# Kernel optimization log

Measured on AMD Instinct MI355X. Metric: run time of the kernel, lower is better.

## Reference

```python
import jax, jax.numpy as jnp
import numpy as np
import math

E = 256          # embed_dim
H = 8            # num_heads
DH = E // H      # head_dim = 32
Q_LEN = 65536
KV_LEN = 65536
K_NBR = 16       # max_memory_len (neighbors per query)


def setup_inputs() -> dict:
    key = jax.random.key(0)
    ks = jax.random.split(key, 8)
    query = jax.random.normal(ks[0], (Q_LEN, E), dtype=jnp.float32)
    key_t = jax.random.normal(ks[1], (KV_LEN, E), dtype=jnp.float32)
    value = jax.random.normal(ks[2], (KV_LEN, E), dtype=jnp.float32)
    index_pair = jax.random.randint(ks[3], (Q_LEN, K_NBR), 0, KV_LEN, dtype=jnp.int64 if jax.config.jax_enable_x64 else jnp.int32)
    # learned params (xavier-ish init for in_proj, zero biases)
    lim = math.sqrt(6.0 / (3 * E + E))
    in_proj_weight = jax.random.uniform(ks[4], (3 * E, E), minval=-lim, maxval=lim, dtype=jnp.float32)
    in_proj_bias = jnp.zeros((3 * E,), dtype=jnp.float32)
    lim2 = math.sqrt(1.0 / E)
    out_proj_weight = jax.random.uniform(ks[5], (E, E), minval=-lim2, maxval=lim2, dtype=jnp.float32)
    out_proj_bias = jnp.zeros((E,), dtype=jnp.float32)
    return {
        "query": query, "key": key_t, "value": value, "index_pair": index_pair,
        "in_proj_weight": in_proj_weight, "in_proj_bias": in_proj_bias,
        "out_proj_weight": out_proj_weight, "out_proj_bias": out_proj_bias,
    }


def reference(query, key, value, index_pair, in_proj_weight, in_proj_bias, out_proj_weight, out_proj_bias):
    tq = query.shape[0]
    # input projections (split rows of packed in_proj_weight)
    q = query @ in_proj_weight[:E].T + in_proj_bias[:E]
    k = key @ in_proj_weight[E:2 * E].T + in_proj_bias[E:2 * E]
    v = value @ in_proj_weight[2 * E:].T + in_proj_bias[2 * E:]
    q = q.reshape(tq, H, DH) / math.sqrt(DH)   # [Q,H,Dh]
    k = k.reshape(-1, H, DH)                    # [N,H,Dh]
    v = v.reshape(-1, H, DH)
    invalid = index_pair < 0                    # [Q,K]
    all_invalid = jnp.all(invalid, axis=-1)     # [Q]
    safe_pair = jnp.clip(index_pair, 0)
    gathered_k = k[safe_pair]                   # [Q,K,H,Dh]
    gathered_v = v[safe_pair]
    weights = jnp.einsum('qhd,qkhd->qkh', q, gathered_k)  # [Q,K,H]
    neg_inf = jnp.asarray(-jnp.inf, weights.dtype)
    weights = jnp.where(invalid[..., None], neg_inf, weights)
    weights = jnp.where(all_invalid[:, None, None], jnp.zeros((), weights.dtype), weights)
    weights = jax.nn.softmax(weights, axis=1)
    weights = jnp.where(invalid[..., None], jnp.zeros((), weights.dtype), weights)
    out = jnp.einsum('qkh,qkhd->qhd', weights, gathered_v).reshape(tq, E)
    out = out @ out_proj_weight.T + out_proj_bias
    return out, weights.sum(axis=-1) / H
```

## Files before the change

kernel.cpp:

```cpp
#include <hip/hip_runtime.h>
#include <hip/hip_fp16.h>

#define QLEN   65536
#define EDIM   256

typedef _Float16 half8 __attribute__((ext_vector_type(8)));
typedef float    f32x4 __attribute__((ext_vector_type(4)));

static const size_t WQKV_OFF = 0;
static const size_t WOUT_OFF = 768u * 256u * 2u;
static const size_t Q_OFF    = WOUT_OFF + 256u * 256u * 2u;
static const size_t K_OFF    = Q_OFF + (size_t)QLEN * EDIM * 2u;
static const size_t V_OFF    = K_OFF + (size_t)QLEN * EDIM * 2u;
static const size_t A_OFF    = V_OFF + (size_t)QLEN * EDIM * 2u;

__global__ void prep_weights(const float* __restrict__ wqkv,
                             const float* __restrict__ wout,
                             __half* __restrict__ dst)
{
  int g = (blockIdx.x * blockDim.x + threadIdx.x) * 4;
  float4 f;
  if (g < 768 * 256) f = *(const float4*)(wqkv + g);
  else               f = *(const float4*)(wout + (g - 768 * 256));
  union { __half h[4]; uint2 u; } c;
  c.h[0] = __float2half(f.x); c.h[1] = __float2half(f.y);
  c.h[2] = __float2half(f.z); c.h[3] = __float2half(f.w);
  *(uint2*)(dst + g) = c.u;
}

template<bool A_F32, bool OUT_F16>
__global__ __launch_bounds__(512)
void gemm_e256v2(const void* __restrict__ A0, const void* __restrict__ A1,
                 const void* __restrict__ A2,
                 const __half* __restrict__ Wbase, const float* __restrict__ bias,
                 float scale0,
                 void* __restrict__ O0, void* __restrict__ O1, void* __restrict__ O2)
{
  __shared__ __half As[2][128][40];
  __shared__ __half Bs[2][256][40];

  const int y = blockIdx.y;
  const void* Ain  = (y == 0) ? A0 : (y == 1) ? A1 : A2;
  void*       Outp = (y == 0) ? O0 : (y == 1) ? O1 : O2;
  const __half* W  = Wbase + (size_t)y * 256 * 256;
  const float* bp  = bias + y * 256;
  const float scale = (y == 0) ? scale0 : 1.0f;

  const int tid  = threadIdx.x;
  const int lane = tid & 63;
  const int wid  = tid >> 6;
  const int wr   = wid >> 2;
  const int wc   = wid & 3;
  const int gm   = blockIdx.x * 128;

  const int ar = tid >> 2, ac = (tid & 3) * 8;
  const int br = tid >> 1, bc = (tid & 1) * 16;

  const int fr = lane & 15;
  const int fo = (lane >> 4) * 8;
  const int fq = lane >> 4;

  f32x4 acc[4][4] = {};

  float4 ra0, ra1;
  uint4  ua;
  uint4  rb0, rb1;

  if (A_F32) {
    const float* src = (const float*)Ain + (size_t)(gm + ar) * 256 + ac;
    ra0 = ((const float4*)src)[0];
    ra1 = ((const float4*)src)[1];
    union { __half h[8]; uint4 u; } t;
    t.h[0]=__float2half(ra0.x); t.h[1]=__float2half(ra0.y);
    t.h[2]=__float2half(ra0.z); t.h[3]=__float2half(ra0.w);
    t.h[4]=__float2half(ra1.x); t.h[5]=__float2half(ra1.y);
    t.h[6]=__float2half(ra1.z); t.h[7]=__float2half(ra1.w);
    *(uint4*)&As[0][ar][ac] = t.u;
  } else {
    const __half* src = (const __half*)Ain + (size_t)(gm + ar) * 256 + ac;
    *(uint4*)&As[0][ar][ac] = *(const uint4*)src;
  }
  {
    const __half* src = W + (size_t)br * 256 + bc;
    *(uint4*)&Bs[0][br][bc]     = ((const uint4*)src)[0];
    *(uint4*)&Bs[0][br][bc + 8] = ((const uint4*)src)[1];
  }

  int cur = 0;
  #pragma unroll
  for (int kc = 0; kc < 8; ++kc, cur ^= 1) {
    if (kc < 7) {
      if (A_F32) {
        const float* src = (const float*)Ain + (size_t)(gm + ar) * 256 + (kc + 1) * 32 + ac;
        ra0 = ((const float4*)src)[0];
        ra1 = ((const float4*)src)[1];
      } else {
        const __half* src = (const __half*)Ain + (size_t)(gm + ar) * 256 + (kc + 1) * 32 + ac;
        ua = *(const uint4*)src;
      }
      const __half* src = W + (size_t)br * 256 + (kc + 1) * 32 + bc;
      rb0 = ((const uint4*)src)[0];
      rb1 = ((const uint4*)src)[1];
    }

    __syncthreads();

    half8 af[4], bf[4];
    #pragma unroll
    for (int i = 0; i < 4; ++i) af[i] = *(const half8*)&As[cur][wr*64 + i*16 + fr][fo];
    #pragma unroll
    for (int j = 0; j < 4; ++j) bf[j] = *(const half8*)&Bs[cur][wc*64 + j*16 + fr][fo];
    #pragma unroll
    for (int i = 0; i < 4; ++i)
      #pragma unroll
      for (int j = 0; j < 4; ++j)
        acc[i][j] = __builtin_amdgcn_mfma_f32_16x16x32_f16(af[i], bf[j], acc[i][j], 0, 0, 0);

    if (kc < 7) {
      if (A_F32) {
        union { __half h[8]; uint4 u; } t;
        t.h[0]=__float2half(ra0.x); t.h[1]=__float2half(ra0.y);
        t.h[2]=__float2half(ra0.z); t.h[3]=__float2half(ra0.w);
        t.h[4]=__float2half(ra1.x); t.h[5]=__float2half(ra1.y);
        t.h[6]=__float2half(ra1.z); t.h[7]=__float2half(ra1.w);
        *(uint4*)&As[cur ^ 1][ar][ac] = t.u;
      } else {
        *(uint4*)&As[cur ^ 1][ar][ac] = ua;
      }
      *(uint4*)&Bs[cur ^ 1][br][bc]     = rb0;
      *(uint4*)&Bs[cur ^ 1][br][bc + 8] = rb1;
    }
  }

  #pragma unroll
  for (int j = 0; j < 4; ++j) {
    const int col = wc*64 + j*16 + fr;
    const float bj = bp[col];
    #pragma unroll
    for (int i = 0; i < 4; ++i) {
      const int row0 = gm + wr*64 + i*16 + fq*4;
      #pragma unroll
      for (int rr = 0; rr < 4; ++rr) {
        const float v = (acc[i][j][rr] + bj) * scale;
        if (OUT_F16) ((__half*)Outp)[(size_t)(row0 + rr) * 256 + col] = __float2half(v);
        else         ((float*) Outp)[(size_t)(row0 + rr) * 256 + col] = v;
      }
    }
  }
}

__global__ __launch_bounds__(256)
void attn_local(const __half* __restrict__ qws, const __half* __restrict__ kws,
                const __half* __restrict__ vws, const int* __restrict__ idxp,
                __half* __restrict__ attn, float* __restrict__ wsum)
{
  const int tid  = threadIdx.x;
  const int lane = tid & 63;
  const int wid  = tid >> 6;
  const int q    = blockIdx.x * 4 + wid;
  const int col  = lane * 4;

  union U2 { uint2 u; __half h[4]; };

  U2 qu; qu.u = *(const uint2*)(qws + (size_t)q * 256 + col);
  const float q0 = __half2float(qu.h[0]), q1 = __half2float(qu.h[1]),
              q2 = __half2float(qu.h[2]), q3 = __half2float(qu.h[3]);

  int myidx = 0;
  if (lane < 16) myidx = idxp[(size_t)q * 16 + lane];

  float logit[16];
  U2 vk[16];
  #pragma unroll
  for (int n = 0; n < 16; ++n) {
    const int kvi = __shfl(myidx, n);
    float p;
    if (kvi >= 0) {
      U2 ku; ku.u = *(const uint2*)(kws + (size_t)kvi * 256 + col);
      vk[n].u     = *(const uint2*)(vws + (size_t)kvi * 256 + col);
      p = q0 * __half2float(ku.h[0]) + q1 * __half2float(ku.h[1])
        + q2 * __half2float(ku.h[2]) + q3 * __half2float(ku.h[3]);
      p += __shfl_xor(p, 1);
      p += __shfl_xor(p, 2);
      p += __shfl_xor(p, 4);
    } else {
      p = -__builtin_inff();
      vk[n].u = make_uint2(0u, 0u);
    }
    logit[n] = p;
  }

  float m = logit[0];
  #pragma unroll
  for (int n = 1; n < 16; ++n) m = fmaxf(m, logit[n]);
  const bool allinv = (m < -1e37f);

  float w[16]; float ssum = 0.f;
  #pragma unroll
  for (int n = 0; n < 16; ++n) {
    const float e = allinv ? 0.f : __expf(logit[n] - m);
    w[n] = e; ssum += e;
  }
  const float inv = allinv ? 0.f : (1.0f / ssum);

  float a0 = 0.f, a1 = 0.f, a2 = 0.f, a3 = 0.f;
  #pragma unroll
  for (int n = 0; n < 16; ++n) {
    const float wn = w[n] * inv;
    w[n] = wn;
    a0 += wn * __half2float(vk[n].h[0]);
    a1 += wn * __half2float(vk[n].h[1]);
    a2 += wn * __half2float(vk[n].h[2]);
    a3 += wn * __half2float(vk[n].h[3]);
  }

  U2 o; o.h[0] = __float2half(a0); o.h[1] = __float2half(a1);
        o.h[2] = __float2half(a2); o.h[3] = __float2half(a3);
  *(uint2*)(attn + (size_t)q * 256 + col) = o.u;

  float wsr = 0.f;
  #pragma unroll
  for (int n = 0; n < 16; ++n) {
    float t = w[n];
    t += __shfl_xor(t, 8);
    t += __shfl_xor(t, 16);
    t += __shfl_xor(t, 32);
    if (lane == n) wsr = t;
  }
  if (lane < 16) wsum[(size_t)q * 16 + lane] = wsr * 0.125f;
}

extern "C" void kernel_launch(void* const* d_in, const int* in_sizes, int n_in,
                              void* d_out, int out_size, void* d_ws, size_t ws_size,
                              hipStream_t stream)
{
  const float* query = (const float*)d_in[0];
  const float* key   = (const float*)d_in[1];
  const float* value = (const float*)d_in[2];
  const int*   idxp  = (const int*)  d_in[3];
  const float* wqkv  = (const float*)d_in[4];
  const float* bqkv  = (const float*)d_in[5];
  const float* wout  = (const float*)d_in[6];
  const float* bout  = (const float*)d_in[7];
  float* out = (float*)d_out;

  char* ws   = (char*)d_ws;
  __half* Wh = (__half*)(ws + WQKV_OFF);
  __half* qh = (__half*)(ws + Q_OFF);
  __half* kh = (__half*)(ws + K_OFF);
  __half* vh = (__half*)(ws + V_OFF);
  __half* ah = (__half*)(ws + A_OFF);

  prep_weights<<<256, 256, 0, stream>>>(wqkv, wout, Wh);

  const float qscale = 0.17677669529663687f;

  gemm_e256v2<true, true><<<dim3(QLEN / 128, 3), 512, 0, stream>>>(
      query, key, value, Wh, bqkv, qscale, qh, kh, vh);

  attn_local<<<QLEN / 4, 256, 0, stream>>>(qh, kh, vh, idxp, ah, out + (size_t)QLEN * EDIM);

  gemm_e256v2<false, false><<<dim3(QLEN / 128, 1), 512, 0, stream>>>(
      ah, ah, ah, Wh + 768 * 256, bout, 1.0f, out, out, out);
}
```

Measured before the change: 452.1 us.

## Restructure neighbor attention with 16-byte gathers and split-wave neighbor halves

The attention kernel now has each wave handle four queries in sequence. Each lane loads 8 halves per gather (uint4) instead of 4, and the two 32-lane halves of the wave process even and odd neighbors in parallel. All K and V gathers are issued up front, with invalid indices clamped to row 0 instead of branched around. This is meant to cut gather instruction count and raise memory-level parallelism. In exchange it adds cross-half shuffles for the max, sum and output reduction, uses more registers, and launches fewer blocks.

```diff
diff --git a/kernel.cpp b/kernel.cpp
--- a/kernel.cpp
+++ b/kernel.cpp
@@ -149,85 +149,102 @@
   }
 }
 
+#define QPW 4
 __global__ __launch_bounds__(256)
-void attn_local(const __half* __restrict__ qws, const __half* __restrict__ kws,
-                const __half* __restrict__ vws, const int* __restrict__ idxp,
-                __half* __restrict__ attn, float* __restrict__ wsum)
+void attn_local2(const __half* __restrict__ qws, const __half* __restrict__ kws,
+                 const __half* __restrict__ vws, const int* __restrict__ idxp,
+                 __half* __restrict__ attn, float* __restrict__ wsum)
 {
   const int tid  = threadIdx.x;
   const int lane = tid & 63;
   const int wid  = tid >> 6;
-  const int q    = blockIdx.x * 4 + wid;
-  const int col  = lane * 4;
-
-  union U2 { uint2 u; __half h[4]; };
-
-  U2 qu; qu.u = *(const uint2*)(qws + (size_t)q * 256 + col);
-  const float q0 = __half2float(qu.h[0]), q1 = __half2float(qu.h[1]),
-              q2 = __half2float(qu.h[2]), q3 = __half2float(qu.h[3]);
-
-  int myidx = 0;
-  if (lane < 16) myidx = idxp[(size_t)q * 16 + lane];
-
-  float logit[16];
-  U2 vk[16];
-  #pragma unroll
-  for (int n = 0; n < 16; ++n) {
-    const int kvi = __shfl(myidx, n);
-    float p;
-    if (kvi >= 0) {
-      U2 ku; ku.u = *(const uint2*)(kws + (size_t)kvi * 256 + col);
-      vk[n].u     = *(const uint2*)(vws + (size_t)kvi * 256 + col);
-      p = q0 * __half2float(ku.h[0]) + q1 * __half2float(ku.h[1])
-        + q2 * __half2float(ku.h[2]) + q3 * __half2float(ku.h[3]);
+  const int l31  = lane & 31;
+  const int half = lane >> 5;
+  const int col  = l31 * 8;
+
+  const int q0 = (blockIdx.x * 4 + wid) * QPW;
+
+  union U4 { uint4 u; __half h[8]; };
+
+  for (int it = 0; it < QPW; ++it) {
+    const int q = q0 + it;
+
+    int myidx = 0;
+    if (lane < 16) myidx = idxp[(size_t)q * 16 + lane];
+
+    U4 qu; qu.u = *(const uint4*)(qws + (size_t)q * 256 + col);
+
+    int kvi[8];
+    U4 ku[8], vu[8];
+    #pragma unroll
+    for (int j = 0; j < 8; ++j) {
+      kvi[j] = __shfl(myidx, 2 * j + half);
+      const size_t s = (size_t)(kvi[j] < 0 ? 0 : kvi[j]) * 256;
+      ku[j].u = *(const uint4*)(kws + s + col);
+    }
+    #pragma unroll
+    for (int j = 0; j < 8; ++j) {
+      const size_t s = (size_t)(kvi[j] < 0 ? 0 : kvi[j]) * 256;
+      vu[j].u = *(const uint4*)(vws + s + col);
+    }
+
+    float qf[8];
+    #pragma unroll
+    for (int e = 0; e < 8; ++e) qf[e] = __half2float(qu.h[e]);
+
+    float logit[8];
+    #pragma unroll
+    for (int j = 0; j < 8; ++j) {
+      float p = 0.f;
+      #pragma unroll
+      for (int e = 0; e < 8; ++e) p += qf[e] * __half2float(ku[j].h[e]);
       p += __shfl_xor(p, 1);
       p += __shfl_xor(p, 2);
-      p += __shfl_xor(p, 4);
-    } else {
-      p = -__builtin_inff();
-      vk[n].u = make_uint2(0u, 0u);
-    }
-    logit[n] = p;
-  }
-
-  float m = logit[0];
-  #pragma unroll
-  for (int n = 1; n < 16; ++n) m = fmaxf(m, logit[n]);
-  const bool allinv = (m < -1e37f);
-
-  float w[16]; float ssum = 0.f;
-  #pragma unroll
-  for (int n = 0; n < 16; ++n) {
-    const float e = allinv ? 0.f : __expf(logit[n] - m);
-    w[n] = e; ssum += e;
-  }
-  const float inv = allinv ? 0.f : (1.0f / ssum);
-
-  float a0 = 0.f, a1 = 0.f, a2 = 0.f, a3 = 0.f;
-  #pragma unroll
-  for (int n = 0; n < 16; ++n) {
-    const float wn = w[n] * inv;
-    w[n] = wn;
-    a0 += wn * __half2float(vk[n].h[0]);
-    a1 += wn * __half2float(vk[n].h[1]);
-    a2 += wn * __half2float(vk[n].h[2]);
-    a3 += wn * __half2float(vk[n].h[3]);
-  }
-
-  U2 o; o.h[0] = __float2half(a0); o.h[1] = __float2half(a1);
-        o.h[2] = __float2half(a2); o.h[3] = __float2half(a3);
-  *(uint2*)(attn + (size_t)q * 256 + col) = o.u;
-
-  float wsr = 0.f;
-  #pragma unroll
-  for (int n = 0; n < 16; ++n) {
-    float t = w[n];
-    t += __shfl_xor(t, 8);
-    t += __shfl_xor(t, 16);
-    t += __shfl_xor(t, 32);
-    if (lane == n) wsr = t;
-  }
-  if (lane < 16) wsum[(size_t)q * 16 + lane] = wsr * 0.125f;
+      logit[j] = (kvi[j] < 0) ? -__builtin_inff() : p;
+    }
+
+    float m = logit[0];
+    #pragma unroll
+    for (int j = 1; j < 8; ++j) m = fmaxf(m, logit[j]);
+    m = fmaxf(m, __shfl_xor(m, 32));
+    const bool allinv = (m < -1e37f);
+
+    float w[8]; float s8 = 0.f;
+    #pragma unroll
+    for (int j = 0; j < 8; ++j) {
+      const float e = allinv ? 0.f : __expf(logit[j] - m);
+      w[j] = e; s8 += e;
+    }
+    const float s = s8 + __shfl_xor(s8, 32);
+    const float inv = allinv ? 0.f : (1.0f / s);
+
+    float acc[8] = {};
+    #pragma unroll
+    for (int j = 0; j < 8; ++j) {
+      const float wn = w[j] * inv;
+      w[j] = wn;
+      #pragma unroll
+      for (int e = 0; e < 8; ++e) acc[e] += wn * __half2float(vu[j].h[e]);
+    }
+
+    #pragma unroll
+    for (int e = 0; e < 8; ++e) acc[e] += __shfl_xor(acc[e], 32);
+    if (half == 0) {
+      U4 o;
+      #pragma unroll
+      for (int e = 0; e < 8; ++e) o.h[e] = __float2half(acc[e]);
+      *(uint4*)(attn + (size_t)q * 256 + col) = o.u;
+    }
+
+    #pragma unroll
+    for (int j = 0; j < 8; ++j) {
+      float t = w[j];
+      t += __shfl_xor(t, 4);
+      t += __shfl_xor(t, 8);
+      t += __shfl_xor(t, 16);
+      if (l31 == j) wsum[(size_t)q * 16 + 2 * j + half] = t * 0.125f;
+    }
+  }
 }
 
 extern "C" void kernel_launch(void* const* d_in, const int* in_sizes, int n_in,
@@ -258,7 +275,8 @@
   gemm_e256v2<true, true><<<dim3(QLEN / 128, 3), 512, 0, stream>>>(
       query, key, value, Wh, bqkv, qscale, qh, kh, vh);
 
-  attn_local<<<QLEN / 4, 256, 0, stream>>>(qh, kh, vh, idxp, ah, out + (size_t)QLEN * EDIM);
+  attn_local2<<<QLEN / 4 / QPW, 256, 0, stream>>>(qh, kh, vh, idxp, ah,
+                                                  out + (size_t)QLEN * EDIM);
 
   gemm_e256v2<false, false><<<dim3(QLEN / 128, 1), 512, 0, stream>>>(
       ah, ah, ah, Wh + 768 * 256, bout, 1.0f, out, out, out);
```

New measurement: 429.7 us. 1.05x faster.
